# Kernel optimization log

Hardware: AMD Instinct MI355X
Metric: run time of the kernel (lower is better)

Reference implementation:

```python
import jax, jax.numpy as jnp
import numpy as np


def setup_inputs() -> dict:
    key = jax.random.key(0)
    ks = jax.random.split(key, 7)
    B, T, I, H, O = 64, 2048, 32, 256, 32
    s = 0.05
    return {
        "x": jax.random.normal(ks[0], (B, T, I), dtype=jnp.float32),
        "W_ih": jax.random.normal(ks[1], (4 * H, I), dtype=jnp.float32) * s,
        "W_hh": jax.random.normal(ks[2], (4 * H, H), dtype=jnp.float32) * s,
        "b_ih": jax.random.normal(ks[3], (4 * H,), dtype=jnp.float32) * s,
        "b_hh": jax.random.normal(ks[4], (4 * H,), dtype=jnp.float32) * s,
        "fc_w": jax.random.normal(ks[5], (O, H), dtype=jnp.float32) * s,
        "fc_b": jax.random.normal(ks[6], (O,), dtype=jnp.float32) * s,
    }


def _lstm(x, W_ih, W_hh, b_ih, b_hh):
    # x: [B,T,I]; PyTorch gate order: i, f, g, o stacked along 4H axis.
    B = x.shape[0]
    H = W_hh.shape[1]
    # Precompute input contributions for all timesteps in one GEMM: [B,T,4H]
    xg = jnp.einsum('bti,gi->btg', x, W_ih) + b_ih + b_hh

    def step(carry, xg_t):
        h, c = carry  # [B,H] each
        gates = xg_t + h @ W_hh.T  # [B,4H]
        i, f, g, o = jnp.split(gates, 4, axis=-1)
        i = jax.nn.sigmoid(i)
        f = jax.nn.sigmoid(f)
        g = jnp.tanh(g)
        o = jax.nn.sigmoid(o)
        c = f * c + i * g
        h = o * jnp.tanh(c)
        return (h, c), h

    h0 = jnp.zeros((B, H), dtype=x.dtype)
    (_, _), hs = jax.lax.scan(step, (h0, h0), jnp.swapaxes(xg, 0, 1))
    return jnp.swapaxes(hs, 0, 1)  # [B,T,H]


def reference(x, W_ih, W_hh, b_ih, b_hh, fc_w, fc_b):
    out = _lstm(x, W_ih, W_hh, b_ih, b_hh)          # [B,T,H]
    # Conv1d(H, O, kernel_size=1) over channel dim == pointwise linear.
    return jnp.einsum('bth,oh->bto', out, fc_w) + fc_b  # [B,T,O]
```

## Files before the change

kernel.cpp:

```cpp
#include <hip/hip_runtime.h>
#include <cstdint>


#define B_  64
#define T_  2048
#define I_  32
#define H_  256
#define G4  1024
#define O_  32

typedef int v16i __attribute__((ext_vector_type(16)));
typedef int v8i  __attribute__((ext_vector_type(8)));
typedef _Float16 h2_t __attribute__((ext_vector_type(2)));

#if __has_builtin(__builtin_amdgcn_sdot4)
__device__ __forceinline__ int dot4(int a, int b, int c) {
    return __builtin_amdgcn_sdot4(a, b, c, false);
}
#else
__device__ __forceinline__ int dot4(int a, int b, int c) {
    c += (int)(int8_t)(a)        * (int)(int8_t)(b);
    c += (int)(int8_t)(a >> 8)   * (int)(int8_t)(b >> 8);
    c += (int)(int8_t)(a >> 16)  * (int)(int8_t)(b >> 16);
    c += (int)(int8_t)(a >> 24)  * (int)(int8_t)(b >> 24);
    return c;
}
#endif

__device__ __forceinline__ float fdot2h(h2_t a, h2_t b, float c) {
#if __has_builtin(__builtin_amdgcn_fdot2)
    return __builtin_amdgcn_fdot2(a, b, c, false);
#else
    return c + (float)a[0] * (float)b[0] + (float)a[1] * (float)b[1];
#endif
}

#define QWHH_OFF 0u
#define QWIH_OFF 262144u
#define S1_OFF   294912u
#define S2_OFF   299008u
#define BIAS_OFF 303104u
#define XQ_OFF   307200u
#define HBUF_OFF 9744384u
#define XREC  72
#define HREC  800
#define HSLOTS 2049

__device__ __forceinline__ uint32_t pack_q(int q0, int q1, int q2, int q3) {
    return  ((uint32_t)(uint8_t)(int8_t)q0)
          | (((uint32_t)(uint8_t)(int8_t)q1) << 8)
          | (((uint32_t)(uint8_t)(int8_t)q2) << 16)
          | (((uint32_t)(uint8_t)(int8_t)q3) << 24);
}
__device__ __forceinline__ int clamp127(int v) {
    return v < -127 ? -127 : (v > 127 ? 127 : v);
}


__global__ __launch_bounds__(64) void prep_w(
    const float* __restrict__ Whh, const float* __restrict__ Wih,
    const float* __restrict__ bih, const float* __restrict__ bhh,
    uint32_t* __restrict__ qwhh, uint32_t* __restrict__ qwih,
    float* __restrict__ s1, float* __restrict__ s2, float* __restrict__ bias)
{
    const int r = blockIdx.x;
    const int l = threadIdx.x;
    const int j = r & 255, g = r >> 8;
    const int col = 64 * (j >> 5) + ((g & 1) ? 32 : 0) + (j & 31);
    const int dbase = (g >= 2) ? 64 : 0;
    const int xbase = (g >= 2) ? 8 : 0;

    const float4 wv = ((const float4*)(Whh + r * H_))[l];
    float m = fmaxf(fmaxf(fabsf(wv.x), fabsf(wv.y)), fmaxf(fabsf(wv.z), fabsf(wv.w)));
    #pragma unroll
    for (int s = 1; s < 64; s <<= 1) m = fmaxf(m, __shfl_xor(m, s, 64));
    const float S1 = fmaxf(m, 1e-20f) / 127.f;

    float xm = (l < I_) ? fabsf(Wih[r * I_ + l]) : 0.f;
    #pragma unroll
    for (int s = 1; s < 64; s <<= 1) xm = fmaxf(xm, __shfl_xor(xm, s, 64));
    const float S2 = fmaxf(xm, 1e-20f) / 127.f;

    {
        const float r1 = 1.f / S1;
        qwhh[(dbase + l) * 512 + col] = pack_q(
            clamp127((int)rintf(wv.x * r1)), clamp127((int)rintf(wv.y * r1)),
            clamp127((int)rintf(wv.z * r1)), clamp127((int)rintf(wv.w * r1)));
    }
    if (l < 8) {
        const float4 xw = ((const float4*)(Wih + r * I_))[l];
        const float r2 = 1.f / S2;
        qwih[(xbase + l) * 512 + col] = pack_q(
            clamp127((int)rintf(xw.x * r2)), clamp127((int)rintf(xw.y * r2)),
            clamp127((int)rintf(xw.z * r2)), clamp127((int)rintf(xw.w * r2)));
    }
    if (l == 0) { s1[r] = S1; s2[r] = S2; bias[r] = bih[r] + bhh[r]; }
}

__global__ __launch_bounds__(256) void prep_x(
    const float* __restrict__ x, char* __restrict__ xq)
{
    __shared__ float xb[64 * 32];
    const int base = blockIdx.x * 64 * 32;
    for (int i = threadIdx.x; i < 2048; i += 256) xb[i] = x[base + i];
    __syncthreads();
    const int t = threadIdx.x;
    if (t < 64) {
        float m = 0.f;
        for (int k = 0; k < 32; k++) m = fmaxf(m, fabsf(xb[t * 32 + k]));
        const float S = fmaxf(m, 1e-20f) / 127.f;
        const float rS = 1.f / S;
        const int row = blockIdx.x * 64 + t;
        uint32_t* rec = (uint32_t*)(xq + (size_t)row * XREC);
        for (int jj = 0; jj < 8; jj++) {
            int qa[4], qb[4];
            for (int e = 0; e < 4; e++) {
                float v = xb[t * 32 + jj * 4 + e] * rS;
                int a = clamp127((int)rintf(v));
                int b = clamp127((int)rintf((v - (float)a) * 127.f));
                qa[e] = a; qb[e] = b;
            }
            rec[jj]     = pack_q(qa[0], qa[1], qa[2], qa[3]);
            rec[8 + jj] = pack_q(qb[0], qb[1], qb[2], qb[3]);
        }
        ((float*)rec)[16] = S;
    }
}

#define GRP(GACC, WOFF, HV, HOFF, SC) { int acc_ = 0; \
    acc_ = dot4((int)w[(WOFF)+0], HV[(HOFF)+0], acc_); \
    acc_ = dot4((int)w[(WOFF)+1], HV[(HOFF)+1], acc_); \
    acc_ = dot4((int)w[(WOFF)+2], HV[(HOFF)+2], acc_); \
    acc_ = dot4((int)w[(WOFF)+3], HV[(HOFF)+3], acc_); \
    acc_ = dot4((int)w[(WOFF)+4], HV[(HOFF)+4], acc_); \
    acc_ = dot4((int)w[(WOFF)+5], HV[(HOFF)+5], acc_); \
    acc_ = dot4((int)w[(WOFF)+6], HV[(HOFF)+6], acc_); \
    acc_ = dot4((int)w[(WOFF)+7], HV[(HOFF)+7], acc_); \
    GACC = fmaf((float)acc_, (SC), GACC); }

__global__
__attribute__((amdgpu_flat_work_group_size(512, 512)))
__attribute__((amdgpu_waves_per_eu(2, 2)))
void lstm_main(
    const uint32_t* __restrict__ qwhh, const uint32_t* __restrict__ qwih,
    const float* __restrict__ s1v, const float* __restrict__ s2v,
    const float* __restrict__ biasv, const char* __restrict__ xq,
    char* __restrict__ hbuf)
{
    const int b   = blockIdx.x;
    const int tid = threadIdx.x;
    const int w_  = tid >> 6, l = tid & 63;
    const int j   = 32 * w_ + (l & 31);
    const bool up = (l >= 32);
    const int rowA = up ? 256 + j : j;
    const int rowB = up ? 768 + j : 512 + j;

    uint32_t w[128];
    #pragma unroll
    for (int d = 0; d < 128; d++) w[d] = qwhh[d * 512 + tid];
    uint32_t wx[16];
    #pragma unroll
    for (int k = 0; k < 16; k++) wx[k] = qwih[k * 512 + tid];

    const float S1A = s1v[rowA], S1B = s1v[rowB];
    const float S2A = s2v[rowA], S2B = s2v[rowB];
    const float biasA = biasv[rowA], biasB = biasv[rowB];

    char* hb = hbuf + (size_t)b * ((size_t)HSLOTS * HREC);
    const char* xb = xq + (size_t)b * T_ * XREC;
    if (tid < 72) ((uint32_t*)hb)[tid] = 0u;
    float c_state = 0.f;
    __syncthreads();

    for (int t = 0; t < T_; t++) {
        const char* hrec = hb + (size_t)t * HREC;
        const char* xrec = xb + (size_t)t * XREC;
        v16i h0, h1, h2, h3, xv; v8i scv; int sxi;
        asm volatile(
            "s_load_dwordx16 %0, %7, 0x0\n\t"
            "s_load_dwordx16 %1, %7, 0x40\n\t"
            "s_load_dwordx16 %2, %7, 0x80\n\t"
            "s_load_dwordx16 %3, %7, 0xc0\n\t"
            "s_load_dwordx8  %4, %7, 0x100\n\t"
            "s_load_dwordx16 %5, %8, 0x0\n\t"
            "s_load_dword    %6, %8, 0x40\n\t"
            "s_waitcnt lgkmcnt(0)"
            : "=&s"(h0), "=&s"(h1), "=&s"(h2), "=&s"(h3), "=&s"(scv),
              "=&s"(xv), "=&s"(sxi)
            : "s"(hrec), "s"(xrec)
            : "memory");

        float gaccA = 0.f, gaccB = 0.f;
        GRP(gaccA,  0, h0, 0, __int_as_float(scv[0]));
        GRP(gaccA,  8, h0, 8, __int_as_float(scv[1]));
        GRP(gaccA, 16, h1, 0, __int_as_float(scv[2]));
        GRP(gaccA, 24, h1, 8, __int_as_float(scv[3]));
        GRP(gaccA, 32, h2, 0, __int_as_float(scv[4]));
        GRP(gaccA, 40, h2, 8, __int_as_float(scv[5]));
        GRP(gaccA, 48, h3, 0, __int_as_float(scv[6]));
        GRP(gaccA, 56, h3, 8, __int_as_float(scv[7]));
        GRP(gaccB,  64, h0, 0, __int_as_float(scv[0]));
        GRP(gaccB,  72, h0, 8, __int_as_float(scv[1]));
        GRP(gaccB,  80, h1, 0, __int_as_float(scv[2]));
        GRP(gaccB,  88, h1, 8, __int_as_float(scv[3]));
        GRP(gaccB,  96, h2, 0, __int_as_float(scv[4]));
        GRP(gaccB, 104, h2, 8, __int_as_float(scv[5]));
        GRP(gaccB, 112, h3, 0, __int_as_float(scv[6]));
        GRP(gaccB, 120, h3, 8, __int_as_float(scv[7]));

        int aA = 0, aL = 0, bA = 0, bL = 0;
        #pragma unroll
        for (int k = 0; k < 8; k++) {
            aA = dot4((int)wx[k],     xv[k],     aA);
            aL = dot4((int)wx[k],     xv[8 + k], aL);
            bA = dot4((int)wx[8 + k], xv[k],     bA);
            bL = dot4((int)wx[8 + k], xv[8 + k], bL);
        }
        const float Sx = __int_as_float(sxi);
        const float xA = ((float)aA + (float)aL * (1.f / 127.f)) * (S2A * Sx) + biasA;
        const float xB = ((float)bA + (float)bL * (1.f / 127.f)) * (S2B * Sx) + biasB;

        const float gateA = gaccA * S1A + xA;
        const float gateB = gaccB * S1B + xB;
        const float gF = __shfl_xor(gateA, 32, 64);
        const float gO = __shfl_xor(gateB, 32, 64);

        char* hw = hb + (size_t)(t + 1) * HREC;
        if (l < 32) {
            const float i_ = 1.f / (1.f + __expf(-gateA));
            const float g_ = 2.f / (1.f + __expf(-2.f * gateB)) - 1.f;
            const float f_ = 1.f / (1.f + __expf(-gF));
            const float o_ = 1.f / (1.f + __expf(-gO));
            c_state = f_ * c_state + i_ * g_;
            const float tc = 2.f / (1.f + __expf(-2.f * c_state)) - 1.f;
            const float hval = o_ * tc;

            float m = fabsf(hval);
            #pragma unroll
            for (int s = 1; s < 32; s <<= 1) m = fmaxf(m, __shfl_xor(m, s, 64));
            m = fmaxf(m, 1e-12f);
            const int q = clamp127((int)rintf(hval * (127.f / m)));

            uint32_t q8 = (uint32_t)q & 0xffu;
            uint32_t p = q8 | (((uint32_t)__shfl_xor((int)q8, 1, 64)) << 8);
            p = p | (((uint32_t)__shfl_xor((int)p, 2, 64)) << 16);
            const uint32_t p4 = (uint32_t)__shfl_xor((int)p, 4, 64);

            union { _Float16 f; uint16_t u; } hc; hc.f = (_Float16)hval;
            uint32_t hh = (uint32_t)hc.u;
            uint32_t hp = hh | (((uint32_t)__shfl_xor((int)hh, 1, 64)) << 16);
            const uint32_t hp2 = (uint32_t)__shfl_xor((int)hp, 2, 64);

            if ((l & 7) == 0) *(uint2*)(hw + 32 * w_ + l) = make_uint2(p, p4);
            if ((l & 3) == 0) *(uint2*)(hw + 288 + 64 * w_ + 2 * l) = make_uint2(hp, hp2);
            if (l == 0) ((float*)(hw + 256))[w_] = m * (1.f / 127.f);
        }
        __syncthreads();
    }
}

__global__ __launch_bounds__(256) void fc_kernel(
    const char* __restrict__ hbuf, const float* __restrict__ fcw,
    const float* __restrict__ fcb, float* __restrict__ out)
{
    __shared__ uint32_t hlds[64 * 128];
    __shared__ uint32_t wlds[32 * 32 * 4];
    const int b  = blockIdx.x >> 5;
    const int t0 = (blockIdx.x & 31) * 64;
    const char* hb = hbuf + (size_t)b * ((size_t)HSLOTS * HREC);

    for (int u = threadIdx.x; u < 2048; u += 256) {
        const int r = u >> 5, c = u & 31;
        ((uint4*)hlds)[u] =
            *(const uint4*)(hb + (size_t)(t0 + r + 1) * HREC + 288 + c * 16);
    }
    for (int i = threadIdx.x; i < 4096; i += 256) {
        const int o = i >> 7, kp = i & 127;
        union { h2_t h; uint32_t u; } cv;
        cv.h[0] = (_Float16)fcw[o * 256 + 2 * kp];
        cv.h[1] = (_Float16)fcw[o * 256 + 2 * kp + 1];
        wlds[((kp >> 2) * 32 + o) * 4 + (kp & 3)] = cv.u;
    }
    __syncthreads();

    const int o = threadIdx.x & 31, rg = threadIdx.x >> 5;
    const float bv = fcb[o];
    float acc[8];
    #pragma unroll
    for (int rr = 0; rr < 8; rr++) acc[rr] = bv;

    for (int ch = 0; ch < 32; ch++) {
        const uint4 wv = *(const uint4*)(wlds + (ch * 32 + o) * 4);
        union { uint32_t u; h2_t h; } w0, w1, w2, w3;
        w0.u = wv.x; w1.u = wv.y; w2.u = wv.z; w3.u = wv.w;
        #pragma unroll
        for (int rr = 0; rr < 8; rr++) {
            const int row = rg * 8 + rr;
            const uint4 hv = *(const uint4*)(hlds + row * 128 + ch * 4);
            union { uint32_t u; h2_t h; } x0, x1, x2, x3;
            x0.u = hv.x; x1.u = hv.y; x2.u = hv.z; x3.u = hv.w;
            float a = acc[rr];
            a = fdot2h(w0.h, x0.h, a);
            a = fdot2h(w1.h, x1.h, a);
            a = fdot2h(w2.h, x2.h, a);
            a = fdot2h(w3.h, x3.h, a);
            acc[rr] = a;
        }
    }
    #pragma unroll
    for (int rr = 0; rr < 8; rr++)
        out[((size_t)b * T_ + t0 + rg * 8 + rr) * O_ + o] = acc[rr];
}

extern "C" void kernel_launch(void* const* d_in, const int* in_sizes, int n_in,
                              void* d_out, int out_size, void* d_ws, size_t ws_size,
                              hipStream_t stream) {
    const float* x    = (const float*)d_in[0];
    const float* Wih  = (const float*)d_in[1];
    const float* Whh  = (const float*)d_in[2];
    const float* bih  = (const float*)d_in[3];
    const float* bhh  = (const float*)d_in[4];
    const float* fcw  = (const float*)d_in[5];
    const float* fcb  = (const float*)d_in[6];
    float* out = (float*)d_out;

    char* ws = (char*)d_ws;
    uint32_t* qwhh = (uint32_t*)(ws + QWHH_OFF);
    uint32_t* qwih = (uint32_t*)(ws + QWIH_OFF);
    float*    s1   = (float*)(ws + S1_OFF);
    float*    s2   = (float*)(ws + S2_OFF);
    float*    bias = (float*)(ws + BIAS_OFF);
    char*     xq   = ws + XQ_OFF;
    char*     hbuf = ws + HBUF_OFF;

    prep_w<<<G4, 64, 0, stream>>>(Whh, Wih, bih, bhh, qwhh, qwih, s1, s2, bias);
    prep_x<<<(B_ * T_) / 64, 256, 0, stream>>>(x, xq);
    lstm_main<<<B_, 512, 0, stream>>>(qwhh, qwih, s1, s2, bias, xq, hbuf);
    fc_kernel<<<(B_ * T_) / 64, 256, 0, stream>>>(hbuf, fcw, fcb, out);
}
```

Measured before the change: 4.081 ms.

## Split LSTM gate rows across 1024 threads with shared-memory gate exchange

The recurrent kernel now runs 1024 threads per sequence, one gate row per thread, each holding 64 weight dwords instead of 128. Gate activations pass through shared memory to the 256 cell-update threads, which needs an extra barrier per timestep. The hidden-state record drops the fp16 copy, so stores per step shrink. The FC kernel instead dequantizes the int8 hidden state into fp16, which adds precision loss and extra work there.

```diff
diff --git a/kernel.cpp b/kernel.cpp
--- a/kernel.cpp
+++ b/kernel.cpp
@@ -10,7 +10,7 @@
 #define O_  32
 
 typedef int v16i __attribute__((ext_vector_type(16)));
-typedef int v8i  __attribute__((ext_vector_type(8)));
+typedef int v4i  __attribute__((ext_vector_type(4)));
 typedef _Float16 h2_t __attribute__((ext_vector_type(2)));
 
 #if __has_builtin(__builtin_amdgcn_sdot4)
@@ -43,7 +43,7 @@
 #define XQ_OFF   307200u
 #define HBUF_OFF 9744384u
 #define XREC  72
-#define HREC  800
+#define HREC  512
 #define HSLOTS 2049
 
 __device__ __forceinline__ uint32_t pack_q(int q0, int q1, int q2, int q3) {
@@ -55,7 +55,6 @@
 __device__ __forceinline__ int clamp127(int v) {
     return v < -127 ? -127 : (v > 127 ? 127 : v);
 }
-
 
 __global__ __launch_bounds__(64) void prep_w(
     const float* __restrict__ Whh, const float* __restrict__ Wih,
@@ -65,10 +64,6 @@
 {
     const int r = blockIdx.x;
     const int l = threadIdx.x;
-    const int j = r & 255, g = r >> 8;
-    const int col = 64 * (j >> 5) + ((g & 1) ? 32 : 0) + (j & 31);
-    const int dbase = (g >= 2) ? 64 : 0;
-    const int xbase = (g >= 2) ? 8 : 0;
 
     const float4 wv = ((const float4*)(Whh + r * H_))[l];
     float m = fmaxf(fmaxf(fabsf(wv.x), fabsf(wv.y)), fmaxf(fabsf(wv.z), fabsf(wv.w)));
@@ -83,14 +78,14 @@
 
     {
         const float r1 = 1.f / S1;
-        qwhh[(dbase + l) * 512 + col] = pack_q(
+        qwhh[l * G4 + r] = pack_q(
             clamp127((int)rintf(wv.x * r1)), clamp127((int)rintf(wv.y * r1)),
             clamp127((int)rintf(wv.z * r1)), clamp127((int)rintf(wv.w * r1)));
     }
     if (l < 8) {
         const float4 xw = ((const float4*)(Wih + r * I_))[l];
         const float r2 = 1.f / S2;
-        qwih[(xbase + l) * 512 + col] = pack_q(
+        qwih[l * G4 + r] = pack_q(
             clamp127((int)rintf(xw.x * r2)), clamp127((int)rintf(xw.y * r2)),
             clamp127((int)rintf(xw.z * r2)), clamp127((int)rintf(xw.w * r2)));
     }
@@ -127,21 +122,26 @@
     }
 }
 
-#define GRP(GACC, WOFF, HV, HOFF, SC) { int acc_ = 0; \
-    acc_ = dot4((int)w[(WOFF)+0], HV[(HOFF)+0], acc_); \
-    acc_ = dot4((int)w[(WOFF)+1], HV[(HOFF)+1], acc_); \
-    acc_ = dot4((int)w[(WOFF)+2], HV[(HOFF)+2], acc_); \
-    acc_ = dot4((int)w[(WOFF)+3], HV[(HOFF)+3], acc_); \
-    acc_ = dot4((int)w[(WOFF)+4], HV[(HOFF)+4], acc_); \
-    acc_ = dot4((int)w[(WOFF)+5], HV[(HOFF)+5], acc_); \
-    acc_ = dot4((int)w[(WOFF)+6], HV[(HOFF)+6], acc_); \
-    acc_ = dot4((int)w[(WOFF)+7], HV[(HOFF)+7], acc_); \
-    GACC = fmaf((float)acc_, (SC), GACC); }
-
-__global__
-__attribute__((amdgpu_flat_work_group_size(512, 512)))
-__attribute__((amdgpu_waves_per_eu(2, 2)))
-void lstm_main(
+#define GRP16(GACC, WOFF, HV, SC) { int a_ = 0; \
+    a_ = dot4((int)w[(WOFF)+0],  HV[0],  a_); \
+    a_ = dot4((int)w[(WOFF)+1],  HV[1],  a_); \
+    a_ = dot4((int)w[(WOFF)+2],  HV[2],  a_); \
+    a_ = dot4((int)w[(WOFF)+3],  HV[3],  a_); \
+    a_ = dot4((int)w[(WOFF)+4],  HV[4],  a_); \
+    a_ = dot4((int)w[(WOFF)+5],  HV[5],  a_); \
+    a_ = dot4((int)w[(WOFF)+6],  HV[6],  a_); \
+    a_ = dot4((int)w[(WOFF)+7],  HV[7],  a_); \
+    a_ = dot4((int)w[(WOFF)+8],  HV[8],  a_); \
+    a_ = dot4((int)w[(WOFF)+9],  HV[9],  a_); \
+    a_ = dot4((int)w[(WOFF)+10], HV[10], a_); \
+    a_ = dot4((int)w[(WOFF)+11], HV[11], a_); \
+    a_ = dot4((int)w[(WOFF)+12], HV[12], a_); \
+    a_ = dot4((int)w[(WOFF)+13], HV[13], a_); \
+    a_ = dot4((int)w[(WOFF)+14], HV[14], a_); \
+    a_ = dot4((int)w[(WOFF)+15], HV[15], a_); \
+    GACC = fmaf((float)a_, (SC), GACC); }
+
+__global__ __launch_bounds__(1024, 4) void lstm_main(
     const uint32_t* __restrict__ qwhh, const uint32_t* __restrict__ qwih,
     const float* __restrict__ s1v, const float* __restrict__ s2v,
     const float* __restrict__ biasv, const char* __restrict__ xq,
@@ -150,38 +150,39 @@
     const int b   = blockIdx.x;
     const int tid = threadIdx.x;
     const int w_  = tid >> 6, l = tid & 63;
-    const int j   = 32 * w_ + (l & 31);
-    const bool up = (l >= 32);
-    const int rowA = up ? 256 + j : j;
-    const int rowB = up ? 768 + j : 512 + j;
-
-    uint32_t w[128];
-    #pragma unroll
-    for (int d = 0; d < 128; d++) w[d] = qwhh[d * 512 + tid];
-    uint32_t wx[16];
-    #pragma unroll
-    for (int k = 0; k < 16; k++) wx[k] = qwih[k * 512 + tid];
-
-    const float S1A = s1v[rowA], S1B = s1v[rowB];
-    const float S2A = s2v[rowA], S2B = s2v[rowB];
-    const float biasA = biasv[rowA], biasB = biasv[rowB];
+    const int g   = w_ >> 2;
+    const int u   = tid & 255;
+
+    __shared__ float gbuf[1024];
+
+    uint32_t w[64];
+    #pragma unroll
+    for (int d = 0; d < 64; d++) w[d] = qwhh[d * G4 + tid];
+    uint32_t wx[8];
+    #pragma unroll
+    for (int k = 0; k < 8; k++) wx[k] = qwih[k * G4 + tid];
+
+    const float S1 = s1v[tid], S2 = s2v[tid], biasr = biasv[tid];
+    const float sA = (g == 2) ? 2.f : 1.f;
+    const float mA = (g == 2) ? 2.f : 1.f;
+    const float cA = (g == 2) ? -1.f : 0.f;
 
     char* hb = hbuf + (size_t)b * ((size_t)HSLOTS * HREC);
     const char* xb = xq + (size_t)b * T_ * XREC;
-    if (tid < 72) ((uint32_t*)hb)[tid] = 0u;
+    if (tid < 68) ((uint32_t*)hb)[tid] = 0u;
     float c_state = 0.f;
     __syncthreads();
 
     for (int t = 0; t < T_; t++) {
         const char* hrec = hb + (size_t)t * HREC;
         const char* xrec = xb + (size_t)t * XREC;
-        v16i h0, h1, h2, h3, xv; v8i scv; int sxi;
+        v16i h0, h1, h2, h3, xv; v4i scv; int sxi;
         asm volatile(
             "s_load_dwordx16 %0, %7, 0x0\n\t"
             "s_load_dwordx16 %1, %7, 0x40\n\t"
             "s_load_dwordx16 %2, %7, 0x80\n\t"
             "s_load_dwordx16 %3, %7, 0xc0\n\t"
-            "s_load_dwordx8  %4, %7, 0x100\n\t"
+            "s_load_dwordx4  %4, %7, 0x100\n\t"
             "s_load_dwordx16 %5, %8, 0x0\n\t"
             "s_load_dword    %6, %8, 0x40\n\t"
             "s_waitcnt lgkmcnt(0)"
@@ -190,69 +191,46 @@
             : "s"(hrec), "s"(xrec)
             : "memory");
 
-        float gaccA = 0.f, gaccB = 0.f;
-        GRP(gaccA,  0, h0, 0, __int_as_float(scv[0]));
-        GRP(gaccA,  8, h0, 8, __int_as_float(scv[1]));
-        GRP(gaccA, 16, h1, 0, __int_as_float(scv[2]));
-        GRP(gaccA, 24, h1, 8, __int_as_float(scv[3]));
-        GRP(gaccA, 32, h2, 0, __int_as_float(scv[4]));
-        GRP(gaccA, 40, h2, 8, __int_as_float(scv[5]));
-        GRP(gaccA, 48, h3, 0, __int_as_float(scv[6]));
-        GRP(gaccA, 56, h3, 8, __int_as_float(scv[7]));
-        GRP(gaccB,  64, h0, 0, __int_as_float(scv[0]));
-        GRP(gaccB,  72, h0, 8, __int_as_float(scv[1]));
-        GRP(gaccB,  80, h1, 0, __int_as_float(scv[2]));
-        GRP(gaccB,  88, h1, 8, __int_as_float(scv[3]));
-        GRP(gaccB,  96, h2, 0, __int_as_float(scv[4]));
-        GRP(gaccB, 104, h2, 8, __int_as_float(scv[5]));
-        GRP(gaccB, 112, h3, 0, __int_as_float(scv[6]));
-        GRP(gaccB, 120, h3, 8, __int_as_float(scv[7]));
-
-        int aA = 0, aL = 0, bA = 0, bL = 0;
+        float gacc = 0.f;
+        GRP16(gacc,  0, h0, __int_as_float(scv[0]));
+        GRP16(gacc, 16, h1, __int_as_float(scv[1]));
+        GRP16(gacc, 32, h2, __int_as_float(scv[2]));
+        GRP16(gacc, 48, h3, __int_as_float(scv[3]));
+
+        int aA = 0, aL = 0;
         #pragma unroll
         for (int k = 0; k < 8; k++) {
-            aA = dot4((int)wx[k],     xv[k],     aA);
-            aL = dot4((int)wx[k],     xv[8 + k], aL);
-            bA = dot4((int)wx[8 + k], xv[k],     bA);
-            bL = dot4((int)wx[8 + k], xv[8 + k], bL);
+            aA = dot4((int)wx[k], xv[k],     aA);
+            aL = dot4((int)wx[k], xv[8 + k], aL);
         }
         const float Sx = __int_as_float(sxi);
-        const float xA = ((float)aA + (float)aL * (1.f / 127.f)) * (S2A * Sx) + biasA;
-        const float xB = ((float)bA + (float)bL * (1.f / 127.f)) * (S2B * Sx) + biasB;
-
-        const float gateA = gaccA * S1A + xA;
-        const float gateB = gaccB * S1B + xB;
-        const float gF = __shfl_xor(gateA, 32, 64);
-        const float gO = __shfl_xor(gateB, 32, 64);
+        const float xc = ((float)aA + (float)aL * (1.f / 127.f)) * (S2 * Sx) + biasr;
+
+        const float gate = gacc * S1 + xc;
+        const float y = fmaf(1.f / (1.f + __expf(-sA * gate)), mA, cA);
+
+        if (g > 0) gbuf[(g << 8) | u] = y;
+        __syncthreads();
 
         char* hw = hb + (size_t)(t + 1) * HREC;
-        if (l < 32) {
-            const float i_ = 1.f / (1.f + __expf(-gateA));
-            const float g_ = 2.f / (1.f + __expf(-2.f * gateB)) - 1.f;
-            const float f_ = 1.f / (1.f + __expf(-gF));
-            const float o_ = 1.f / (1.f + __expf(-gO));
-            c_state = f_ * c_state + i_ * g_;
+        if (g == 0) {
+            const float yf = gbuf[256 + tid];
+            const float yg = gbuf[512 + tid];
+            const float yo = gbuf[768 + tid];
+            c_state = yf * c_state + y * yg;
             const float tc = 2.f / (1.f + __expf(-2.f * c_state)) - 1.f;
-            const float hval = o_ * tc;
+            const float hval = yo * tc;
 
             float m = fabsf(hval);
             #pragma unroll
-            for (int s = 1; s < 32; s <<= 1) m = fmaxf(m, __shfl_xor(m, s, 64));
+            for (int s = 1; s < 64; s <<= 1) m = fmaxf(m, __shfl_xor(m, s, 64));
             m = fmaxf(m, 1e-12f);
             const int q = clamp127((int)rintf(hval * (127.f / m)));
 
             uint32_t q8 = (uint32_t)q & 0xffu;
             uint32_t p = q8 | (((uint32_t)__shfl_xor((int)q8, 1, 64)) << 8);
             p = p | (((uint32_t)__shfl_xor((int)p, 2, 64)) << 16);
-            const uint32_t p4 = (uint32_t)__shfl_xor((int)p, 4, 64);
-
-            union { _Float16 f; uint16_t u; } hc; hc.f = (_Float16)hval;
-            uint32_t hh = (uint32_t)hc.u;
-            uint32_t hp = hh | (((uint32_t)__shfl_xor((int)hh, 1, 64)) << 16);
-            const uint32_t hp2 = (uint32_t)__shfl_xor((int)hp, 2, 64);
-
-            if ((l & 7) == 0) *(uint2*)(hw + 32 * w_ + l) = make_uint2(p, p4);
-            if ((l & 3) == 0) *(uint2*)(hw + 288 + 64 * w_ + 2 * l) = make_uint2(hp, hp2);
+            if ((l & 3) == 0) *(uint32_t*)(hw + tid) = p;
             if (l == 0) ((float*)(hw + 256))[w_] = m * (1.f / 127.f);
         }
         __syncthreads();
@@ -269,10 +247,27 @@
     const int t0 = (blockIdx.x & 31) * 64;
     const char* hb = hbuf + (size_t)b * ((size_t)HSLOTS * HREC);
 
-    for (int u = threadIdx.x; u < 2048; u += 256) {
-        const int r = u >> 5, c = u & 31;
-        ((uint4*)hlds)[u] =
-            *(const uint4*)(hb + (size_t)(t0 + r + 1) * HREC + 288 + c * 16);
+    {
+        const int rec = threadIdx.x >> 2, g4 = threadIdx.x & 3;
+        const char* rp = hb + (size_t)(t0 + rec + 1) * HREC;
+        const float sc = *(const float*)(rp + 256 + 4 * g4);
+        #pragma unroll
+        for (int qq = 0; qq < 4; qq++) {
+            const uint4 d = *(const uint4*)(rp + 64 * g4 + 16 * qq);
+            uint32_t vals[4] = {d.x, d.y, d.z, d.w};
+            #pragma unroll
+            for (int e = 0; e < 4; e++) {
+                const uint32_t v = vals[e];
+                union { h2_t h; uint32_t u; } p0, p1;
+                p0.h[0] = (_Float16)((float)(int)(int8_t)(v)       * sc);
+                p0.h[1] = (_Float16)((float)(int)(int8_t)(v >> 8)  * sc);
+                p1.h[0] = (_Float16)((float)(int)(int8_t)(v >> 16) * sc);
+                p1.h[1] = (_Float16)((float)(int)(int8_t)(v >> 24) * sc);
+                const int di = rec * 128 + g4 * 32 + qq * 8 + e * 2;
+                hlds[di]     = p0.u;
+                hlds[di + 1] = p1.u;
+            }
+        }
     }
     for (int i = threadIdx.x; i < 4096; i += 256) {
         const int o = i >> 7, kp = i & 127;
@@ -295,8 +290,8 @@
         w0.u = wv.x; w1.u = wv.y; w2.u = wv.z; w3.u = wv.w;
         #pragma unroll
         for (int rr = 0; rr < 8; rr++) {
-            const int row = rg * 8 + rr;
-            const uint4 hv = *(const uint4*)(hlds + row * 128 + ch * 4);
+            const int rowi = rg * 8 + rr;
+            const uint4 hv = *(const uint4*)(hlds + rowi * 128 + ch * 4);
             union { uint32_t u; h2_t h; } x0, x1, x2, x3;
             x0.u = hv.x; x1.u = hv.y; x2.u = hv.z; x3.u = hv.w;
             float a = acc[rr];
@@ -335,6 +330,6 @@
 
     prep_w<<<G4, 64, 0, stream>>>(Whh, Wih, bih, bhh, qwhh, qwih, s1, s2, bias);
     prep_x<<<(B_ * T_) / 64, 256, 0, stream>>>(x, xq);
-    lstm_main<<<B_, 512, 0, stream>>>(qwhh, qwih, s1, s2, bias, xq, hbuf);
+    lstm_main<<<B_, 1024, 0, stream>>>(qwhh, qwih, s1, s2, bias, xq, hbuf);
     fc_kernel<<<(B_ * T_) / 64, 256, 0, stream>>>(hbuf, fcw, fcb, out);
 }
```

Measured after the change: 3.686 ms. -9.7%, faster.
